# Optimization experiments

Measured on AMD Instinct MI355X. Metric: run time of the kernel, lower is better.

The kernel has to match this reference:

```python
import jax, jax.numpy as jnp
import numpy as np

N_CLASS = 126
C = N_CLASS + 2      # START tag = C-2, STOP tag = C-1
B, T = 128, 512
NEG_BIG = -100000.0  # transition mask value from the torch init
NEG_INIT = -10000.0  # alpha init value


def setup_inputs() -> dict:
    key = jax.random.key(0)
    k1, k2, k3, k4 = jax.random.split(key, 4)
    feats = jax.random.normal(k1, (B, T, C), dtype=jnp.float32)
    # contiguous prefix masks (valid lengths in [1, T]) as the CRF scoring assumes
    lengths = jax.random.randint(k2, (B,), 1, T + 1)
    mask = (jnp.arange(T)[None, :] < lengths[:, None]).astype(jnp.int32)
    tags = jax.random.randint(k3, (B, T), 0, N_CLASS)  # real tags exclude START/STOP
    trans = jax.random.normal(k4, (C, C), dtype=jnp.float32)
    trans = trans.at[:, C - 2].set(NEG_BIG)  # nothing transitions INTO start
    trans = trans.at[C - 1, :].set(NEG_BIG)  # nothing transitions OUT of stop
    return {"feats": feats, "mask": mask, "tags": tags, "transitions": trans}


def _forward_alg_batch(feats, mask, trans):
    # log-partition via (logsumexp, +) semiring scan over time
    Bc, Tc, Cc = feats.shape
    alpha0 = jnp.full((Bc, Cc), NEG_INIT, feats.dtype).at[:, Cc - 2].set(0.0)
    maskb = mask.astype(bool)

    def step(alpha, xs):
        feat_t, m_t = xs                                   # [B,C], [B]
        smat = alpha[:, :, None] + feat_t[:, None, :] + trans[None]  # [B,C,C]: i->j
        new = jax.nn.logsumexp(smat, axis=1)               # [B,C]
        return jnp.where(m_t[:, None], new, alpha), None

    alpha, _ = jax.lax.scan(
        step, alpha0, (jnp.swapaxes(feats, 0, 1), jnp.swapaxes(maskb, 0, 1))
    )
    last = jax.nn.logsumexp(alpha + trans[:, Cc - 1][None, :], axis=1)  # to STOP
    return jnp.sum(last)


def _score_sentence_batch(feats, tags, mask, trans):
    Bc, Tc, Cc = feats.shape
    seq_len = mask.astype(jnp.int32).sum(1)                # [B]
    r = jnp.arange(Bc)
    start = jnp.full((Bc, 1), Cc - 2, tags.dtype)
    stop = jnp.full((Bc, 1), Cc - 1, tags.dtype)
    pad_start = jnp.concatenate([start, tags], axis=1)     # [B,T+1]
    pad_stop = jnp.concatenate([tags, stop], axis=1)       # [B,T+1]
    pad_stop = pad_stop.at[r, seq_len].set(Cc - 1)         # transition to STOP at end
    t = trans[pad_start, pad_stop]                          # [B,T+1]
    t_score = jnp.sum(jnp.cumsum(t, axis=1)[r, seq_len])
    f = jnp.take_along_axis(feats, tags[:, :, None], axis=2)[..., 0]  # [B,T]
    f_score = jnp.sum(jnp.where(mask.astype(bool), f, 0.0))
    return t_score + f_score


def reference(feats, mask, tags, transitions):
    # CRFTagger.calculate_loss with use_crf=True: NLL / batch_size
    nll = _forward_alg_batch(feats, mask, transitions) - _score_sentence_batch(
        feats, tags, mask, transitions
    )
    return nll / feats.shape[0]
```

## Files before the change

### kernel.cpp

```cpp
#include <hip/hip_runtime.h>


#define BB   128
#define TT   512
#define CC   128
#define NTHR 128
#define PF   4
#define WS_STRIDE 320

typedef float v2f __attribute__((ext_vector_type(2)));

__device__ __forceinline__ void bar_nodrain() {
    asm volatile("s_waitcnt lgkmcnt(0)\n\ts_barrier" ::: "memory");
}

#define R32(X) X(0) X(1) X(2) X(3) X(4) X(5) X(6) X(7) \
               X(8) X(9) X(10) X(11) X(12) X(13) X(14) X(15) \
               X(16) X(17) X(18) X(19) X(20) X(21) X(22) X(23) \
               X(24) X(25) X(26) X(27) X(28) X(29) X(30) X(31)

template<int DIR>
__device__ __forceinline__ void scan_body(
    const float* __restrict__ feats,
    const int*   __restrict__ mask,
    const int*   __restrict__ tags,
    const float* __restrict__ trans,
    float*       __restrict__ ws,
    float      (*buf)[CC],
    float*       wred)
{
    const int bb  = blockIdx.x >> 1;
    const int tid = threadIdx.x;
    const int j   = tid;
    const int wv  = tid >> 6;
    const int base = bb * TT;

    int mv[4];
    #pragma unroll
    for (int c = 0; c < 4; ++c) mv[c] = mask[base + c * NTHR + tid];
    int len = 0;
    #pragma unroll
    for (int c = 0; c < 4; ++c) len += __syncthreads_count(mv[c]);

    if (DIR == 0) {
        float sc = 0.0f;
        #pragma unroll
        for (int c = 0; c < 4; ++c) {
            const int t = c * NTHR + tid;
            if (mv[c]) {
                const int tg = tags[base + t];
                sc += feats[((size_t)(base + t)) * CC + tg];
                sc += (t == 0) ? trans[(CC - 2) * CC + tg]
                               : trans[tags[base + t - 1] * CC + tg];
                const int nm = (t == TT - 1) ? 0 : mask[base + t + 1];
                if (!nm) sc += trans[tg * CC + (CC - 1)];
            }
        }
        #pragma unroll
        for (int o = 1; o <= 32; o <<= 1) sc += __shfl_xor(sc, o);
        if ((tid & 63) == 0) wred[wv] = sc;
        __syncthreads();
        if (tid == 0) ws[16 + (size_t)bb * WS_STRIDE + 258] = wred[0] + wred[1];
    }

#define DECLF(q) v2f Ea_##q, Eb_##q;
    R32(DECLF)
#undef DECLF
#define INITF(q) \
    if (DIR == 0) { \
        const float t0 = trans[(size_t)(4 * q    ) * CC + j]; \
        const float t1 = trans[(size_t)(4 * q + 1) * CC + j]; \
        const float t2 = trans[(size_t)(4 * q + 2) * CC + j]; \
        const float t3 = trans[(size_t)(4 * q + 3) * CC + j]; \
        Ea_##q.x = __expf(t0); Ea_##q.y = __expf(t1); \
        Eb_##q.x = __expf(t2); Eb_##q.y = __expf(t3); \
    } else { \
        const float4 u = *(const float4*)&trans[(size_t)j * CC + 4 * q]; \
        Ea_##q.x = __expf(u.x); Ea_##q.y = __expf(u.y); \
        Eb_##q.x = __expf(u.z); Eb_##q.y = __expf(u.w); \
    }
    R32(INITF)
#undef INITF

    const float* fb = feats + (size_t)base * CC;
    const int M      = len >> 1;
    const int nB     = len - M;
    const int nSteps = DIR ? nB : M;

    if (DIR == 0) {
        buf[0][j] = (j == CC - 2) ? 1.0f : 0.0f;
    } else {
        buf[0][j] = __expf(trans[(size_t)j * CC + (CC - 1)])
                  * __expf(fb[(size_t)(len - 1) * CC + j]);
    }

    float fx[PF];
    #pragma unroll
    for (int k = 0; k < PF; ++k) {
        int tg = DIR ? (len - 2 - k) : k;
        tg = (tg > 0) ? tg : 0;
        fx[k] = fb[(size_t)tg * CC + j];
    }

    bar_nodrain();

    float S = 0.0f;
    const int nUp = (nSteps + 3) & ~3;

    for (int tc = 0; tc < nUp; tc += 4) {
        #pragma unroll
        for (int k = 0; k < 4; ++k) {
            const int it  = tc + k;
            const int par = k & 1;
            const float4* qp = (const float4*)&buf[par][0];

            v2f a0 = {0.f, 0.f}, a1 = {0.f, 0.f};
            float u0val = 1.0f;
#define DOTF(q) { \
            const float4 P = qp[q]; \
            if (q == 0) u0val = P.x; \
            v2f U01; U01.x = P.x; U01.y = P.y; \
            v2f U23; U23.x = P.z; U23.y = P.w; \
            a0 = __builtin_elementwise_fma(Ea_##q, U01, a0); \
            a1 = __builtin_elementwise_fma(Eb_##q, U23, a1); \
        }
            R32(DOTF)
#undef DOTF
            a0 += a1;
            const float s = a0.x + a0.y;

            const bool noMul = (DIR != 0) && (it == nSteps - 1);
            const float ef = noMul ? 1.0f : __expf(fx[k]);

            float v;
            if (k == 3) {
                v = ef * s * __builtin_amdgcn_rcpf(u0val);
            } else {
                v = ef * s;
            }

            int tn = DIR ? (len - 2 - (it + PF)) : (it + PF);
            tn = DIR ? ((tn > 0) ? tn : 0) : ((tn < TT) ? tn : (TT - 1));
            fx[k] = fb[(size_t)tn * CC + j];

            if (it < nSteps) {
                if (k == 3) S += __logf(u0val);
                buf[par ^ 1][j] = v;
            }
            bar_nodrain();
        }
    }

    float* resv = ws + 16 + (size_t)bb * WS_STRIDE + DIR * 128;
    resv[j] = buf[nSteps & 1][j];
    if (tid == 0) ws[16 + (size_t)bb * WS_STRIDE + 256 + DIR] = S;
}

__global__ __launch_bounds__(NTHR, 1) void crf_scan(
    const float* __restrict__ feats,
    const int*   __restrict__ mask,
    const int*   __restrict__ tags,
    const float* __restrict__ trans,
    float*       __restrict__ ws)
{
    __shared__ __align__(16) float buf[2][CC];
    __shared__ float wred[2];
    if (blockIdx.x & 1) scan_body<1>(feats, mask, tags, trans, ws, buf, wred);
    else                scan_body<0>(feats, mask, tags, trans, ws, buf, wred);
}

__global__ void crf_epi(const float* __restrict__ ws, float* __restrict__ out)
{
    const int lane = threadIdx.x;
    float r = 0.0f;
    #pragma unroll
    for (int h = 0; h < 2; ++h) {
        const int b = lane * 2 + h;
        const float* base = ws + 16 + (size_t)b * WS_STRIDE;
        float dot = 0.0f;
        #pragma unroll 8
        for (int i = 0; i < 128; i += 4) {
            const float4 av = *(const float4*)&base[i];
            const float4 bv = *(const float4*)&base[128 + i];
            dot += av.x * bv.x + av.y * bv.y + av.z * bv.z + av.w * bv.w;
        }
        r += __logf(dot) + base[256] + base[257] - base[258];
    }
    #pragma unroll
    for (int o = 1; o <= 32; o <<= 1) r += __shfl_xor(r, o);
    if (lane == 0) out[0] = r * (1.0f / (float)BB);
}

extern "C" void kernel_launch(void* const* d_in, const int* in_sizes, int n_in,
                              void* d_out, int out_size, void* d_ws, size_t ws_size,
                              hipStream_t stream)
{
    const float* feats = (const float*)d_in[0];
    const int*   mask  = (const int*)d_in[1];
    const int*   tags  = (const int*)d_in[2];
    const float* trans = (const float*)d_in[3];
    float* out = (float*)d_out;
    float* ws  = (float*)d_ws;

    crf_scan<<<BB * 2, NTHR, 0, stream>>>(feats, mask, tags, trans, ws);
    crf_epi<<<1, 64, 0, stream>>>(ws, out);
}
```

Measured before the change: 197.9 us.

## Split each scan step across 512 threads with 16-lane teams and DPP reductions

Each block grows from 128 to 512 threads. Every 16-lane team computes four output tags, each lane handling an 8-row slice of the transition matrix, and partial sums are combined with DPP cross-lane adds. This shortens the serial per-step dot product from 128 FMAs per thread to a few FMAs plus a reduction, so the latency of the sequential time scan drops. In exchange there are more warps per barrier, an extra reduction on every step, and fewer registers holding the exponentiated transitions.

```diff
diff --git a/kernel.cpp b/kernel.cpp
--- a/kernel.cpp
+++ b/kernel.cpp
@@ -4,7 +4,7 @@
 #define BB   128
 #define TT   512
 #define CC   128
-#define NTHR 128
+#define NTHR 512
 #define PF   4
 #define WS_STRIDE 320
 
@@ -14,10 +14,19 @@
     asm volatile("s_waitcnt lgkmcnt(0)\n\ts_barrier" ::: "memory");
 }
 
-#define R32(X) X(0) X(1) X(2) X(3) X(4) X(5) X(6) X(7) \
-               X(8) X(9) X(10) X(11) X(12) X(13) X(14) X(15) \
-               X(16) X(17) X(18) X(19) X(20) X(21) X(22) X(23) \
-               X(24) X(25) X(26) X(27) X(28) X(29) X(30) X(31)
+template<int CTRL>
+__device__ __forceinline__ float dpp_xadd(float x) {
+    const int y = __builtin_amdgcn_update_dpp(0, __float_as_int(x), CTRL, 0xF, 0xF, true);
+    return x + __int_as_float(y);
+}
+
+__device__ __forceinline__ float red16(float x) {
+    x = dpp_xadd<0xB1>(x);
+    x = dpp_xadd<0x4E>(x);
+    x = dpp_xadd<0x141>(x);
+    x = dpp_xadd<0x140>(x);
+    return x;
+}
 
 template<int DIR>
 __device__ __forceinline__ void scan_body(
@@ -29,80 +38,105 @@
     float      (*buf)[CC],
     float*       wred)
 {
-    const int bb  = blockIdx.x >> 1;
-    const int tid = threadIdx.x;
-    const int j   = tid;
-    const int wv  = tid >> 6;
-    const int base = bb * TT;
-
-    int mv[4];
-    #pragma unroll
-    for (int c = 0; c < 4; ++c) mv[c] = mask[base + c * NTHR + tid];
-    int len = 0;
-    #pragma unroll
-    for (int c = 0; c < 4; ++c) len += __syncthreads_count(mv[c]);
+    const int bb   = blockIdx.x >> 1;
+    const int tid  = threadIdx.x;
+    const int team = tid >> 4;
+    const int sub  = tid & 15;
+    const int j0   = team * 4;
+    const int wid  = tid >> 6;
+
+    const int myM = mask[bb * TT + tid];
+    const int len = __syncthreads_count(myM);
 
     if (DIR == 0) {
         float sc = 0.0f;
+        if (myM) {
+            const int tg = tags[bb * TT + tid];
+            sc += feats[((size_t)(bb * TT + tid)) * CC + tg];
+            sc += (tid == 0) ? trans[(CC - 2) * CC + tg]
+                             : trans[tags[bb * TT + tid - 1] * CC + tg];
+            const int nm = (tid == TT - 1) ? 0 : mask[bb * TT + tid + 1];
+            if (!nm) sc += trans[tg * CC + (CC - 1)];
+        }
+        #pragma unroll
+        for (int o = 1; o <= 32; o <<= 1) sc += __shfl_xor(sc, o);
+        if ((tid & 63) == 0) wred[wid] = sc;
+        __syncthreads();
+        if (tid == 0) {
+            float s = 0.0f;
+            #pragma unroll
+            for (int k = 0; k < 8; ++k) s += wred[k];
+            ws[16 + (size_t)bb * WS_STRIDE + 258] = s;
+        }
+    }
+
+    const int cA = 2 * sub + (sub >> 3);
+    const int cB = 2 * sub + 1 - (sub >> 3);
+    const int rA = cA * 4;
+    const int rB = cB * 4;
+
+    v2f EA[4], EA2[4], EB[4], EB2[4];
+    if (DIR == 0) {
+        const float4 a0 = *(const float4*)&trans[(size_t)(rA    ) * CC + j0];
+        const float4 a1 = *(const float4*)&trans[(size_t)(rA + 1) * CC + j0];
+        const float4 a2 = *(const float4*)&trans[(size_t)(rA + 2) * CC + j0];
+        const float4 a3 = *(const float4*)&trans[(size_t)(rA + 3) * CC + j0];
+        const float4 b0 = *(const float4*)&trans[(size_t)(rB    ) * CC + j0];
+        const float4 b1 = *(const float4*)&trans[(size_t)(rB + 1) * CC + j0];
+        const float4 b2 = *(const float4*)&trans[(size_t)(rB + 2) * CC + j0];
+        const float4 b3 = *(const float4*)&trans[(size_t)(rB + 3) * CC + j0];
+        const float* p0 = (const float*)&a0; const float* p1 = (const float*)&a1;
+        const float* p2 = (const float*)&a2; const float* p3 = (const float*)&a3;
+        const float* q0 = (const float*)&b0; const float* q1 = (const float*)&b1;
+        const float* q2 = (const float*)&b2; const float* q3 = (const float*)&b3;
         #pragma unroll
         for (int c = 0; c < 4; ++c) {
-            const int t = c * NTHR + tid;
-            if (mv[c]) {
-                const int tg = tags[base + t];
-                sc += feats[((size_t)(base + t)) * CC + tg];
-                sc += (t == 0) ? trans[(CC - 2) * CC + tg]
-                               : trans[tags[base + t - 1] * CC + tg];
-                const int nm = (t == TT - 1) ? 0 : mask[base + t + 1];
-                if (!nm) sc += trans[tg * CC + (CC - 1)];
-            }
-        }
-        #pragma unroll
-        for (int o = 1; o <= 32; o <<= 1) sc += __shfl_xor(sc, o);
-        if ((tid & 63) == 0) wred[wv] = sc;
-        __syncthreads();
-        if (tid == 0) ws[16 + (size_t)bb * WS_STRIDE + 258] = wred[0] + wred[1];
-    }
-
-#define DECLF(q) v2f Ea_##q, Eb_##q;
-    R32(DECLF)
-#undef DECLF
-#define INITF(q) \
-    if (DIR == 0) { \
-        const float t0 = trans[(size_t)(4 * q    ) * CC + j]; \
-        const float t1 = trans[(size_t)(4 * q + 1) * CC + j]; \
-        const float t2 = trans[(size_t)(4 * q + 2) * CC + j]; \
-        const float t3 = trans[(size_t)(4 * q + 3) * CC + j]; \
-        Ea_##q.x = __expf(t0); Ea_##q.y = __expf(t1); \
-        Eb_##q.x = __expf(t2); Eb_##q.y = __expf(t3); \
-    } else { \
-        const float4 u = *(const float4*)&trans[(size_t)j * CC + 4 * q]; \
-        Ea_##q.x = __expf(u.x); Ea_##q.y = __expf(u.y); \
-        Eb_##q.x = __expf(u.z); Eb_##q.y = __expf(u.w); \
-    }
-    R32(INITF)
-#undef INITF
-
-    const float* fb = feats + (size_t)base * CC;
+            v2f e;
+            e.x = __expf(p0[c]); e.y = __expf(p1[c]); EA[c]  = e;
+            e.x = __expf(p2[c]); e.y = __expf(p3[c]); EA2[c] = e;
+            e.x = __expf(q0[c]); e.y = __expf(q1[c]); EB[c]  = e;
+            e.x = __expf(q2[c]); e.y = __expf(q3[c]); EB2[c] = e;
+        }
+    } else {
+        #pragma unroll
+        for (int c = 0; c < 4; ++c) {
+            const float4 ua = *(const float4*)&trans[(size_t)(j0 + c) * CC + rA];
+            const float4 ub = *(const float4*)&trans[(size_t)(j0 + c) * CC + rB];
+            v2f e;
+            e.x = __expf(ua.x); e.y = __expf(ua.y); EA[c]  = e;
+            e.x = __expf(ua.z); e.y = __expf(ua.w); EA2[c] = e;
+            e.x = __expf(ub.x); e.y = __expf(ub.y); EB[c]  = e;
+            e.x = __expf(ub.z); e.y = __expf(ub.w); EB2[c] = e;
+        }
+    }
+
+    const float* fb = feats + (size_t)(bb * TT) * CC;
     const int M      = len >> 1;
     const int nB     = len - M;
     const int nSteps = DIR ? nB : M;
 
-    if (DIR == 0) {
-        buf[0][j] = (j == CC - 2) ? 1.0f : 0.0f;
-    } else {
-        buf[0][j] = __expf(trans[(size_t)j * CC + (CC - 1)])
-                  * __expf(fb[(size_t)(len - 1) * CC + j]);
-    }
-
-    float fx[PF];
+    if (tid < CC) {
+        if (DIR == 0) {
+            buf[0][tid] = (tid == CC - 2) ? 1.0f : 0.0f;
+        } else {
+            buf[0][tid] = __expf(trans[(size_t)tid * CC + (CC - 1)])
+                        * __expf(fb[(size_t)(len - 1) * CC + tid]);
+        }
+    }
+
+    float4 fx[PF];
     #pragma unroll
     for (int k = 0; k < PF; ++k) {
         int tg = DIR ? (len - 2 - k) : k;
         tg = (tg > 0) ? tg : 0;
-        fx[k] = fb[(size_t)tg * CC + j];
-    }
-
-    bar_nodrain();
+        fx[k] = *(const float4*)&fb[(size_t)tg * CC + j0];
+    }
+
+    const char* bufc = (const char*)&buf[0][0];
+    const float4* qA0 = (const float4*)(bufc + cA * 16);
+    const float4* qB0 = (const float4*)(bufc + cB * 16);
+    const float4* qA1 = (const float4*)(bufc + CC * 4 + cA * 16);
+    const float4* qB1 = (const float4*)(bufc + CC * 4 + cB * 16);
 
     float S = 0.0f;
     const int nUp = (nSteps + 3) & ~3;
@@ -112,51 +146,65 @@
         for (int k = 0; k < 4; ++k) {
             const int it  = tc + k;
             const int par = k & 1;
-            const float4* qp = (const float4*)&buf[par][0];
-
-            v2f a0 = {0.f, 0.f}, a1 = {0.f, 0.f};
-            float u0val = 1.0f;
-#define DOTF(q) { \
-            const float4 P = qp[q]; \
-            if (q == 0) u0val = P.x; \
-            v2f U01; U01.x = P.x; U01.y = P.y; \
-            v2f U23; U23.x = P.z; U23.y = P.w; \
-            a0 = __builtin_elementwise_fma(Ea_##q, U01, a0); \
-            a1 = __builtin_elementwise_fma(Eb_##q, U23, a1); \
-        }
-            R32(DOTF)
-#undef DOTF
-            a0 += a1;
-            const float s = a0.x + a0.y;
+            bar_nodrain();
+            const float4 P = *(par ? qA1 : qA0);
+            const float4 Q = *(par ? qB1 : qB0);
+            float cval = 1.0f;
+            if (k == 3) cval = buf[1][0];
+
+            v2f U01; U01.x = P.x; U01.y = P.y;
+            v2f U23; U23.x = P.z; U23.y = P.w;
+            v2f V01; V01.x = Q.x; V01.y = Q.y;
+            v2f V23; V23.x = Q.z; V23.y = Q.w;
+
+            float s[4];
+            #pragma unroll
+            for (int c = 0; c < 4; ++c) {
+                v2f acc = {0.f, 0.f};
+                acc = __builtin_elementwise_fma(EA[c],  U01, acc);
+                acc = __builtin_elementwise_fma(EA2[c], U23, acc);
+                acc = __builtin_elementwise_fma(EB[c],  V01, acc);
+                acc = __builtin_elementwise_fma(EB2[c], V23, acc);
+                s[c] = red16(acc.x + acc.y);
+            }
 
             const bool noMul = (DIR != 0) && (it == nSteps - 1);
-            const float ef = noMul ? 1.0f : __expf(fx[k]);
-
-            float v;
+            const float* fxp = (const float*)&fx[k];
+            float v[4];
             if (k == 3) {
-                v = ef * s * __builtin_amdgcn_rcpf(u0val);
+                const float rinv = __builtin_amdgcn_rcpf(cval);
+                #pragma unroll
+                for (int c = 0; c < 4; ++c)
+                    v[c] = (noMul ? 1.0f : __expf(fxp[c])) * s[c] * rinv;
             } else {
-                v = ef * s;
+                #pragma unroll
+                for (int c = 0; c < 4; ++c)
+                    v[c] = (noMul ? 1.0f : __expf(fxp[c])) * s[c];
             }
 
             int tn = DIR ? (len - 2 - (it + PF)) : (it + PF);
             tn = DIR ? ((tn > 0) ? tn : 0) : ((tn < TT) ? tn : (TT - 1));
-            fx[k] = fb[(size_t)tn * CC + j];
+            fx[k] = *(const float4*)&fb[(size_t)tn * CC + j0];
 
             if (it < nSteps) {
-                if (k == 3) S += __logf(u0val);
-                buf[par ^ 1][j] = v;
+                if (k == 3) S += __logf(cval);
+                if (sub == 0) {
+                    float4 w4;
+                    w4.x = v[0]; w4.y = v[1]; w4.z = v[2]; w4.w = v[3];
+                    *(float4*)&buf[par ^ 1][j0] = w4;
+                }
             }
-            bar_nodrain();
-        }
-    }
-
+        }
+    }
+
+    bar_nodrain();
     float* resv = ws + 16 + (size_t)bb * WS_STRIDE + DIR * 128;
-    resv[j] = buf[nSteps & 1][j];
+    if (sub == 0)
+        *(float4*)&resv[j0] = *(const float4*)&buf[nSteps & 1][j0];
     if (tid == 0) ws[16 + (size_t)bb * WS_STRIDE + 256 + DIR] = S;
 }
 
-__global__ __launch_bounds__(NTHR, 1) void crf_scan(
+__global__ __launch_bounds__(NTHR) void crf_scan(
     const float* __restrict__ feats,
     const int*   __restrict__ mask,
     const int*   __restrict__ tags,
@@ -164,7 +212,7 @@
     float*       __restrict__ ws)
 {
     __shared__ __align__(16) float buf[2][CC];
-    __shared__ float wred[2];
+    __shared__ float wred[8];
     if (blockIdx.x & 1) scan_body<1>(feats, mask, tags, trans, ws, buf, wred);
     else                scan_body<0>(feats, mask, tags, trans, ws, buf, wred);
 }
```

After: 183.6 us. 7.2% less time.
